# Kernel tuning notes

Measured on AMD Instinct MI355X. Metric: run time of the kernel, lower is better.

The kernel has to match this reference:

```python
import jax, jax.numpy as jnp
import numpy as np

B, S, E, H, L, DFF = 2, 2048, 512, 8, 2, 2048
D = E // H
EPS = 1e-5


def layernorm(x, g, b):
    mu = jnp.mean(x, axis=-1, keepdims=True)
    var = jnp.var(x, axis=-1, keepdims=True)
    return (x - mu) * jax.lax.rsqrt(var + EPS) * g + b


def layernorm_noaffine(x):
    mu = jnp.mean(x, axis=-1, keepdims=True)
    var = jnp.var(x, axis=-1, keepdims=True)
    return (x - mu) * jax.lax.rsqrt(var + EPS)


def setup_inputs() -> dict:
    key = jax.random.key(0)
    ks = jax.random.split(key, 16)
    s = 0.02
    inp = {
        "x": jax.random.normal(ks[0], (B, S, E), dtype=jnp.float32),
        "mask": jax.random.randint(ks[1], (B, S), 0, 2) == 1,
        # per-layer attention projections, stacked over layers
        "wq": jax.random.normal(ks[2], (L, E, E), dtype=jnp.float32) * s,
        "bq": jnp.zeros((L, E), dtype=jnp.float32),
        "wk": jax.random.normal(ks[3], (L, E, E), dtype=jnp.float32) * s,
        "bk": jnp.zeros((L, E), dtype=jnp.float32),
        "wv": jax.random.normal(ks[4], (L, E, E), dtype=jnp.float32) * s,
        "bv": jnp.zeros((L, E), dtype=jnp.float32),
        # shared norms (module defines a single norm1/norm2 used by every layer)
        "g1": jnp.ones((E,), dtype=jnp.float32),
        "b1": jnp.zeros((E,), dtype=jnp.float32),
        "g2": jnp.ones((E,), dtype=jnp.float32),
        "b2": jnp.zeros((E,), dtype=jnp.float32),
        "gf": jnp.ones((E,), dtype=jnp.float32),
        "bf": jnp.zeros((E,), dtype=jnp.float32),
        # shared Dense FFN (single self.dense used after every layer)
        "W1": jax.random.normal(ks[5], (DFF, E), dtype=jnp.float32) * s,
        "B1": jnp.zeros((DFF,), dtype=jnp.float32),
        "W2": jax.random.normal(ks[6], (E, DFF), dtype=jnp.float32) * s,
        "B2": jnp.zeros((E,), dtype=jnp.float32),
    }
    return inp


def _forward(x, wq, bq, wk, bk, wv, bv, g1, b1, g2, b2, gf, bf, W1, B1, W2, B2, mask):
    scale = 1.0 / jnp.sqrt(jnp.float32(D))
    m = mask[:, None, None, :]  # [B,1,1,S] key padding mask, True = pad
    neg_inf = jnp.float32(-jnp.inf)
    for i in range(L):
        h = layernorm(x, g1, b1)  # norm1(x), used for q,k,v
        q = (h @ wq[i].T + bq[i]).reshape(B, S, H, D).transpose(0, 2, 1, 3)
        k = (h @ wk[i].T + bk[i]).reshape(B, S, H, D).transpose(0, 2, 1, 3)
        v = (h @ wv[i].T + bv[i]).reshape(B, S, H, D).transpose(0, 2, 1, 3)
        logits = jnp.einsum("bhqd,bhkd->bhqk", q, k) * scale
        att = jax.nn.softmax(jnp.where(m, neg_inf, logits), axis=-1)
        att = jnp.where(m, 0.0, att)
        out = jnp.einsum("bhqk,bhkd->bhqd", att, v)
        out = out.transpose(0, 2, 1, 3).reshape(B, S, E)
        x = x + layernorm(out, g2, b2)
        # Dense: LayerNorm(no affine) -> Linear -> ReLU -> Linear, residual
        d = layernorm_noaffine(x)
        d = jax.nn.relu(d @ W1.T + B1)
        d = d @ W2.T + B2
        x = x + d
    return layernorm(x, gf, bf)


def reference(x, mask, wq, bq, wk, bk, wv, bv, g1, b1, g2, b2, gf, bf, W1, B1, W2, B2):
    return _forward(x, wq, bq, wk, bk, wv, bv, g1, b1, g2, b2, gf, bf, W1, B1, W2, B2, mask)
```

## Files before the change

kernel.cpp:

```cpp
#include <hip/hip_runtime.h>
#include <hip/hip_bf16.h>

constexpr int BB   = 2;
constexpr int SS   = 2048;
constexpr int EE   = 512;
constexpr int HH   = 8;
constexpr int DD   = 64;
constexpr int DFF_ = 2048;
constexpr int NTOK = BB * SS;
constexpr int NE   = NTOK * EE;
constexpr float EPSF  = 1e-5f;
constexpr float SCL2  = 0.125f * 1.44269504088896f;
constexpr float MBIAS = -1e30f;
constexpr int KSPLIT = 2;
constexpr int KHALF  = SS / KSPLIT;

typedef __bf16 v8bf __attribute__((ext_vector_type(8)));
typedef __bf16 v4bf __attribute__((ext_vector_type(4)));
typedef float  v4f  __attribute__((ext_vector_type(4)));
typedef unsigned int v4u __attribute__((ext_vector_type(4)));

__device__ __forceinline__ float bf2f(unsigned short u) {
    return __uint_as_float(((unsigned int)u) << 16);
}
__device__ __forceinline__ float bf2f(__bf16 u) {
    unsigned short us = __builtin_bit_cast(unsigned short, u);
    return __uint_as_float(((unsigned int)us) << 16);
}
__device__ __forceinline__ float ldA(const void* p, size_t i, int f) {
    return f ? ((const float*)p)[i] : bf2f(((const unsigned short*)p)[i]);
}
__device__ __forceinline__ void gll16(const void* g, void* l) {
    __builtin_amdgcn_global_load_lds(
        (const __attribute__((address_space(1))) void*)g,
        (__attribute__((address_space(3))) void*)l, 16, 0, 0);
}
__device__ __forceinline__ unsigned cvtpk(float a, float b) {
    unsigned r;
    asm("v_cvt_pk_bf16_f32 %0, %1, %2" : "=v"(r) : "v"(a), "v"(b));
    return r;
}

__global__ __launch_bounds__(256) void cvt_ln(
    const void* __restrict__ in, float* __restrict__ X,
    const void* __restrict__ g, const void* __restrict__ b,
    __bf16* __restrict__ Hb, int* __restrict__ flagw)
{
    const int row = blockIdx.x, t = threadIdx.x;
    __shared__ float red[8], st[2];
    __shared__ int scnt[4], sflag;
    {
        const unsigned short* u = (const unsigned short*)in;
        int bad = 0;
        #pragma unroll
        for (int i = 0; i < 2; ++i) {
            float v = bf2f(u[t + 256 * i]);
            if (!(fabsf(v) < 1000.f)) bad++;
        }
        #pragma unroll
        for (int off = 32; off > 0; off >>= 1) bad += __shfl_down(bad, off, 64);
        if ((t & 63) == 0) scnt[t >> 6] = bad;
        __syncthreads();
        if (t == 0) sflag = (scnt[0] + scnt[1] + scnt[2] + scnt[3] > 1) ? 1 : 0;
        __syncthreads();
    }
    const int f = sflag;
    if (row == 0 && t == 0) *flagw = f;

    const size_t i0 = (size_t)row * EE + t, i1 = i0 + 256;
    float v0 = ldA(in, i0, f);
    float v1 = ldA(in, i1, f);
    float s = v0 + v1, q = v0 * v0 + v1 * v1;
    #pragma unroll
    for (int off = 32; off > 0; off >>= 1) {
        s += __shfl_down(s, off, 64);
        q += __shfl_down(q, off, 64);
    }
    const int wid = t >> 6;
    if ((t & 63) == 0) { red[wid] = s; red[4 + wid] = q; }
    __syncthreads();
    if (t == 0) {
        float S_ = red[0] + red[1] + red[2] + red[3];
        float Q_ = red[4] + red[5] + red[6] + red[7];
        float mu = S_ / EE;
        st[0] = mu;
        st[1] = rsqrtf(Q_ / EE - mu * mu + EPSF);
    }
    __syncthreads();
    const float mu = st[0], rs = st[1];
    float o0 = (v0 - mu) * rs * ldA(g, t, f)       + ldA(b, t, f);
    float o1 = (v1 - mu) * rs * ldA(g, t + 256, f) + ldA(b, t + 256, f);
    X[i0] = v0; X[i1] = v1;
    Hb[i0] = (__bf16)o0; Hb[i1] = (__bf16)o1;
}

__global__ void wcvt_all(const void* __restrict__ wq, const void* __restrict__ wk,
                         const void* __restrict__ wv, const void* __restrict__ W1,
                         const void* __restrict__ W2, __bf16* __restrict__ out,
                         const int* __restrict__ flagp) {
    const int f = *flagp;
    const int i = (blockIdx.x * blockDim.x + threadIdx.x) * 8;
    constexpr int n1 = 2 * EE * EE;
    constexpr int nf = DFF_ * EE;
    const void* src; int off;
    if      (i < n1)          { src = wq; off = i; }
    else if (i < 2 * n1)      { src = wk; off = i - n1; }
    else if (i < 3 * n1)      { src = wv; off = i - 2 * n1; }
    else if (i < 3 * n1 + nf) { src = W1; off = i - 3 * n1; }
    else                      { src = W2; off = i - 3 * n1 - nf; }
    if (f) {
        const float* p = (const float*)src + off;
        #pragma unroll
        for (int j = 0; j < 8; ++j) out[i + j] = (__bf16)p[j];
    } else {
        *(uint4*)(out + i) = *(const uint4*)((const unsigned short*)src + off);
    }
}

__global__ __launch_bounds__(256) void ln_kernel(
    const float* __restrict__ src,
    const void* __restrict__ g, const void* __restrict__ b,
    __bf16* __restrict__ dstb, void* __restrict__ outp,
    const int* __restrict__ flagp)
{
    const int f = *flagp;
    const int row = blockIdx.x, t = threadIdx.x;
    const float* x = src + (size_t)row * EE;
    float v0 = x[t], v1 = x[t + 256];
    float s = v0 + v1, q = v0 * v0 + v1 * v1;
    #pragma unroll
    for (int off = 32; off > 0; off >>= 1) {
        s += __shfl_down(s, off, 64);
        q += __shfl_down(q, off, 64);
    }
    __shared__ float red[8], st[2];
    const int wid = t >> 6;
    if ((t & 63) == 0) { red[wid] = s; red[4 + wid] = q; }
    __syncthreads();
    if (t == 0) {
        float S_ = red[0] + red[1] + red[2] + red[3];
        float Q_ = red[4] + red[5] + red[6] + red[7];
        float mu = S_ / EE;
        st[0] = mu;
        st[1] = rsqrtf(Q_ / EE - mu * mu + EPSF);
    }
    __syncthreads();
    const float mu = st[0], rs = st[1];
    float o0 = (v0 - mu) * rs, o1 = (v1 - mu) * rs;
    if (g) {
        o0 = o0 * ldA(g, t, f)       + ldA(b, t, f);
        o1 = o1 * ldA(g, t + 256, f) + ldA(b, t + 256, f);
    }
    const size_t i0 = (size_t)row * EE + t, i1 = i0 + 256;
    if (dstb) { dstb[i0] = (__bf16)o0; dstb[i1] = (__bf16)o1; }
    if (outp) {
        if (f) { ((float*)outp)[i0] = o0; ((float*)outp)[i1] = o1; }
        else {
            ((__hip_bfloat16*)outp)[i0] = __float2bfloat16(o0);
            ((__hip_bfloat16*)outp)[i1] = __float2bfloat16(o1);
        }
    }
}

__global__ __launch_bounds__(256) void combine_ln(
    const __bf16* __restrict__ Opart, const float* __restrict__ MLl,
    const void* __restrict__ g2, const void* __restrict__ b2,
    float* __restrict__ X, __bf16* __restrict__ Hb,
    const int* __restrict__ flagp)
{
    const int f = *flagp;
    const int tok = blockIdx.x, t = threadIdx.x;
    const int b = tok >> 11, s_ = tok & 2047;
    __shared__ float cinv[8];
    __shared__ float red[8], st[2];
    if (t < 8) {
        float l = 0.f;
        #pragma unroll
        for (int zz = 0; zz < KSPLIT; ++zz)
            l += MLl[(size_t)(zz * 16 + b * 8 + t) * SS + s_];
        cinv[t] = (l > 0.f) ? 1.f / l : 0.f;
    }
    __syncthreads();
    float a0 = 0.f, a1 = 0.f;
    {
        int c = t, h = c >> 6, d = c & 63;
        #pragma unroll
        for (int zz = 0; zz < KSPLIT; ++zz)
            a0 += bf2f(Opart[((size_t)(zz * 16 + b * 8 + h) * SS + s_) * 64 + d]);
        a0 *= cinv[h];
        c = t + 256; h = c >> 6; d = c & 63;
        #pragma unroll
        for (int zz = 0; zz < KSPLIT; ++zz)
            a1 += bf2f(Opart[((size_t)(zz * 16 + b * 8 + h) * SS + s_) * 64 + d]);
        a1 *= cinv[h];
    }
    const int wid = t >> 6;
    {
        float s = a0 + a1, q = a0 * a0 + a1 * a1;
        #pragma unroll
        for (int off = 32; off > 0; off >>= 1) {
            s += __shfl_down(s, off, 64);
            q += __shfl_down(q, off, 64);
        }
        if ((t & 63) == 0) { red[wid] = s; red[4 + wid] = q; }
    }
    __syncthreads();
    if (t == 0) {
        float S_ = red[0] + red[1] + red[2] + red[3];
        float Q_ = red[4] + red[5] + red[6] + red[7];
        float mu = S_ / EE;
        st[0] = mu;
        st[1] = rsqrtf(Q_ / EE - mu * mu + EPSF);
    }
    __syncthreads();
    const float mu1 = st[0], rs1 = st[1];
    const size_t i0 = (size_t)tok * EE + t, i1 = i0 + 256;
    float l0v = (a0 - mu1) * rs1 * ldA(g2, t, f)       + ldA(b2, t, f);
    float l1v = (a1 - mu1) * rs1 * ldA(g2, t + 256, f) + ldA(b2, t + 256, f);
    float x0 = X[i0] + l0v, x1 = X[i1] + l1v;
    __syncthreads();
    {
        float s = x0 + x1, q = x0 * x0 + x1 * x1;
        #pragma unroll
        for (int off = 32; off > 0; off >>= 1) {
            s += __shfl_down(s, off, 64);
            q += __shfl_down(q, off, 64);
        }
        if ((t & 63) == 0) { red[wid] = s; red[4 + wid] = q; }
    }
    __syncthreads();
    if (t == 0) {
        float S_ = red[0] + red[1] + red[2] + red[3];
        float Q_ = red[4] + red[5] + red[6] + red[7];
        float mu = S_ / EE;
        st[0] = mu;
        st[1] = rsqrtf(Q_ / EE - mu * mu + EPSF);
    }
    __syncthreads();
    const float mu2 = st[0], rs2 = st[1];
    X[i0] = x0; X[i1] = x1;
    Hb[i0] = (__bf16)((x0 - mu2) * rs2);
    Hb[i1] = (__bf16)((x1 - mu2) * rs2);
}

__global__ __launch_bounds__(256) void gemm_mfma(
    const __bf16* __restrict__ A,
    const __bf16* Wa, const __bf16* Wb, const __bf16* Wc,
    const void* ba, const void* bb, const void* bc,
    __bf16* oa, __bf16* ob, __bf16* oc,
    float* __restrict__ Cf,
    int M, int N, int K, int flags,
    size_t welem_off, size_t belem_off, const int* __restrict__ flagp)
{
    const int f = *flagp;
    const int z = blockIdx.z;
    const __bf16* W = (z == 0) ? Wa : (z == 1) ? Wb : Wc;
    const void* bias = (z == 0) ? ba : (z == 1) ? bb : bc;
    __bf16* Cb = (z == 0) ? oa : (z == 1) ? ob : oc;
    W += welem_off;
    int kbeg = 0, kend = K;
    if (flags & 4) {
        const int ks = K >> 2;
        kbeg = z * ks; kend = kbeg + ks;
        if (z != 0) bias = nullptr;
    }

    __shared__ __bf16 As[2][128 * 64];
    __shared__ __bf16 Bs[2][128 * 64];
    const int t = threadIdx.x;
    const int w = t >> 6, lane = t & 63;
    const int quad = lane >> 4, l16 = lane & 15;
    const int wr = w >> 1, wc = w & 1;
    const int bm = blockIdx.x * 128, bn = blockIdx.y * 128;

    v4f acc[4][4] = {};

    #define STAGE_TILE(dst, src, rowbase, kk)                                   \
        _Pragma("unroll")                                                       \
        for (int ii = 0; ii < 4; ++ii) {                                        \
            const int c  = t + 256 * ii;                                        \
            const int r  = c >> 3, cc = c & 7;                                  \
            const int es = ((cc ^ (r & 7)) * 8);                                \
            gll16(src + (size_t)(rowbase + r) * K + kk + es,                    \
                  (char*)(dst) + c * 16);                                       \
        }

    STAGE_TILE(As[0], A, bm, kbeg)
    STAGE_TILE(Bs[0], W, bn, kbeg)

    int p = 0;
    for (int k0 = kbeg; k0 < kend; k0 += 64) {
        __syncthreads();
        if (k0 + 64 < kend) {
            const int kn = k0 + 64, q_ = p ^ 1;
            STAGE_TILE(As[q_], A, bm, kn)
            STAGE_TILE(Bs[q_], W, bn, kn)
        }
        #pragma unroll
        for (int ks = 0; ks < 2; ++ks) {
            v8bf af[4], bfr[4];
            #pragma unroll
            for (int i = 0; i < 4; ++i) {
                const int row = wr * 64 + i * 16 + l16;
                const int ph  = (quad + ks * 4) ^ (row & 7);
                af[i] = *(const v8bf*)&As[p][row * 64 + ph * 8];
            }
            #pragma unroll
            for (int j = 0; j < 4; ++j) {
                const int row = wc * 64 + j * 16 + l16;
                const int ph  = (quad + ks * 4) ^ (row & 7);
                bfr[j] = *(const v8bf*)&Bs[p][row * 64 + ph * 8];
            }
            #pragma unroll
            for (int i = 0; i < 4; ++i)
                #pragma unroll
                for (int j = 0; j < 4; ++j)
                    acc[i][j] = __builtin_amdgcn_mfma_f32_16x16x32_bf16(
                        af[i], bfr[j], acc[i][j], 0, 0, 0);
        }
        p ^= 1;
    }
    #undef STAGE_TILE

    float bvv[4];
    #pragma unroll
    for (int j = 0; j < 4; ++j) {
        int col = bn + wc * 64 + j * 16 + l16;
        bvv[j] = bias ? ldA(bias, belem_off + col, f) : 0.f;
    }

    #pragma unroll
    for (int i = 0; i < 4; ++i) {
        const int rowb = bm + wr * 64 + i * 16 + quad * 4;
        #pragma unroll
        for (int j = 0; j < 4; ++j) {
            const int col = bn + wc * 64 + j * 16 + l16;
            #pragma unroll
            for (int r = 0; r < 4; ++r) {
                float v = acc[i][j][r] + bvv[j];
                if (flags & 1) v = fmaxf(v, 0.f);
                const size_t idx = (size_t)(rowb + r) * N + col;
                if (flags & 4)      unsafeAtomicAdd(&Cf[idx], v);
                else if (flags & 2) Cf[idx] += v;
                else                Cb[idx] = (__bf16)v;
            }
        }
    }
}

__global__ __launch_bounds__(256) void gemm_qkv(
    const __bf16* __restrict__ A,
    const __bf16* Wa, const __bf16* Wb, const __bf16* Wc,
    const void* ba, const void* bb, const void* bc,
    __bf16* oa, __bf16* ob, __bf16* oc,
    size_t welem_off, size_t belem_off, const int* __restrict__ flagp)
{
    const int f = *flagp;
    const int z = blockIdx.z;
    const __bf16* W = (z == 0) ? Wa : (z == 1) ? Wb : Wc;
    const void* bias = (z == 0) ? ba : (z == 1) ? bb : bc;
    __bf16* Cb = (z == 0) ? oa : (z == 1) ? ob : oc;
    W += welem_off;
    constexpr int K = EE, N = EE;

    __shared__ __bf16 As[2][128 * 64];
    __shared__ __bf16 Bs[2][64 * 64];
    const int t = threadIdx.x;
    const int w = t >> 6, lane = t & 63;
    const int quad = lane >> 4, l16 = lane & 15;
    const int bm = blockIdx.x * 128, bn = blockIdx.y * 64;

    v4f acc[2][4] = {};

    #define STAGE_A(dst, kk)                                                    \
        _Pragma("unroll")                                                       \
        for (int ii = 0; ii < 4; ++ii) {                                        \
            const int c  = t + 256 * ii;                                        \
            const int r  = c >> 3, cc = c & 7;                                  \
            const int es = ((cc ^ (r & 7)) * 8);                                \
            gll16(A + (size_t)(bm + r) * K + kk + es, (char*)(dst) + c * 16);   \
        }
    #define STAGE_B(dst, kk)                                                    \
        _Pragma("unroll")                                                       \
        for (int ii = 0; ii < 2; ++ii) {                                        \
            const int c  = t + 256 * ii;                                        \
            const int r  = c >> 3, cc = c & 7;                                  \
            const int es = ((cc ^ (r & 7)) * 8);                                \
            gll16(W + (size_t)(bn + r) * K + kk + es, (char*)(dst) + c * 16);   \
        }

    STAGE_A(As[0], 0)
    STAGE_B(Bs[0], 0)

    int p = 0;
    for (int k0 = 0; k0 < K; k0 += 64) {
        __syncthreads();
        if (k0 + 64 < K) {
            const int kn = k0 + 64, q_ = p ^ 1;
            STAGE_A(As[q_], kn)
            STAGE_B(Bs[q_], kn)
        }
        #pragma unroll
        for (int ks = 0; ks < 2; ++ks) {
            v8bf af[2], bfr[4];
            #pragma unroll
            for (int i = 0; i < 2; ++i) {
                const int row = w * 32 + i * 16 + l16;
                const int ph  = (quad + ks * 4) ^ (row & 7);
                af[i] = *(const v8bf*)&As[p][row * 64 + ph * 8];
            }
            #pragma unroll
            for (int j = 0; j < 4; ++j) {
                const int row = j * 16 + l16;
                const int ph  = (quad + ks * 4) ^ (row & 7);
                bfr[j] = *(const v8bf*)&Bs[p][row * 64 + ph * 8];
            }
            #pragma unroll
            for (int i = 0; i < 2; ++i)
                #pragma unroll
                for (int j = 0; j < 4; ++j)
                    acc[i][j] = __builtin_amdgcn_mfma_f32_16x16x32_bf16(
                        af[i], bfr[j], acc[i][j], 0, 0, 0);
        }
        p ^= 1;
    }
    #undef STAGE_A
    #undef STAGE_B

    float bvv[4];
    #pragma unroll
    for (int j = 0; j < 4; ++j) {
        int col = bn + j * 16 + l16;
        bvv[j] = bias ? ldA(bias, belem_off + col, f) : 0.f;
    }

    if (z == 2) {
        #pragma unroll
        for (int i = 0; i < 2; ++i) {
            const int row0 = bm + w * 32 + i * 16 + quad * 4;
            const int b_ = row0 >> 11, sl = row0 & 2047;
            const int s64 = sl & ~63, sloc = sl & 63;
            const int slot = (sloc & 32) + ((sloc >> 2) & 3) * 8 + ((sloc >> 4) & 1) * 4;
            #pragma unroll
            for (int j = 0; j < 4; ++j) {
                const int col = bn + j * 16 + l16;
                const int h_ = col >> 6, d_ = col & 63;
                v4bf u;
                #pragma unroll
                for (int r = 0; r < 4; ++r) u[r] = (__bf16)(acc[i][j][r] + bvv[j]);
                *(v4bf*)(Cb + ((size_t)((b_ * 8 + h_) * 64 + d_)) * SS + s64 + slot) = u;
            }
        }
        return;
    }

    #pragma unroll
    for (int i = 0; i < 2; ++i) {
        const int rowb = bm + w * 32 + i * 16 + quad * 4;
        #pragma unroll
        for (int j = 0; j < 4; ++j) {
            const int col = bn + j * 16 + l16;
            #pragma unroll
            for (int r = 0; r < 4; ++r) {
                const size_t idx = (size_t)(rowb + r) * N + col;
                Cb[idx] = (__bf16)(acc[i][j][r] + bvv[j]);
            }
        }
    }
}

__global__ __launch_bounds__(256) void attn_mfma(
    const __bf16* __restrict__ Qg, const __bf16* __restrict__ Kg,
    const __bf16* __restrict__ Vtg, const int* __restrict__ mask,
    __bf16* __restrict__ Opart, float* __restrict__ MLl)
{
    __shared__ __bf16 Ks[64][72];
    __shared__ __bf16 Vs[64][72];
    __shared__ float  mkf[64];

    const int t = threadIdx.x;
    const int w = t >> 6, lane = t & 63;
    const int quad = lane >> 4, l16 = lane & 15;
    const int bh = blockIdx.y, b = bh >> 3, hh = bh & 7;
    const int q0 = blockIdx.x * 128;
    const int z  = blockIdx.z;
    const int kof = z * KHALF;

    const __bf16* qrow0 = Qg + ((size_t)(b * SS + q0 + w * 32 + l16)) * EE + hh * DD + quad * 8;
    const __bf16* qrow1 = qrow0 + (size_t)16 * EE;
    const v8bf qa00 = *(const v8bf*)qrow0;
    const v8bf qa01 = *(const v8bf*)(qrow0 + 32);
    const v8bf qa10 = *(const v8bf*)qrow1;
    const v8bf qa11 = *(const v8bf*)(qrow1 + 32);

    const int lr = t >> 2, lc = (t & 3) * 16;
    const __bf16* kbase = Kg  + ((size_t)(b * SS + kof + lr)) * EE + hh * DD + lc;
    const __bf16* vbase = Vtg + ((size_t)((b * 8 + hh) * 64 + lr)) * SS + kof + lc;

    v8bf ka0 = *(const v8bf*)kbase, ka1 = *(const v8bf*)(kbase + 8);
    v8bf va0 = *(const v8bf*)vbase, va1 = *(const v8bf*)(vbase + 8);
    float mb = 0.f;
    if (t < 64) mb = mask[b * SS + kof + t] ? MBIAS : 0.f;

    float l0 = 0.f, l1 = 0.f;
    v4f o0[4] = {}, o1[4] = {};

    #pragma unroll 1
    for (int k0 = 0; k0 < KHALF; k0 += 64) {
        *(v8bf*)&Ks[lr][lc]     = ka0;
        *(v8bf*)&Ks[lr][lc + 8] = ka1;
        *(v8bf*)&Vs[lr][lc]     = va0;
        *(v8bf*)&Vs[lr][lc + 8] = va1;
        if (t < 64) mkf[t] = mb;
        __syncthreads();
        if (k0 + 64 < KHALF) {
            ka0 = *(const v8bf*)(kbase + (size_t)(k0 + 64) * EE);
            ka1 = *(const v8bf*)(kbase + (size_t)(k0 + 64) * EE + 8);
            va0 = *(const v8bf*)(vbase + (k0 + 64));
            va1 = *(const v8bf*)(vbase + (k0 + 64) + 8);
            if (t < 64) mb = mask[b * SS + kof + k0 + 64 + t] ? MBIAS : 0.f;
        }

        v4f s0[4], s1[4];
        __builtin_amdgcn_s_setprio(1);
        #pragma unroll
        for (int j = 0; j < 4; ++j) {
            v8bf kf0 = *(const v8bf*)&Ks[j * 16 + l16][quad * 8];
            v8bf kf1 = *(const v8bf*)&Ks[j * 16 + l16][32 + quad * 8];
            v4f za = {}, zb = {};
            za = __builtin_amdgcn_mfma_f32_16x16x32_bf16(kf0, qa00, za, 0, 0, 0);
            za = __builtin_amdgcn_mfma_f32_16x16x32_bf16(kf1, qa01, za, 0, 0, 0);
            zb = __builtin_amdgcn_mfma_f32_16x16x32_bf16(kf0, qa10, zb, 0, 0, 0);
            zb = __builtin_amdgcn_mfma_f32_16x16x32_bf16(kf1, qa11, zb, 0, 0, 0);
            s0[j] = za; s1[j] = zb;
        }
        __builtin_amdgcn_s_setprio(0);
        float4 mk4[4];
        #pragma unroll
        for (int j = 0; j < 4; ++j) mk4[j] = *(const float4*)&mkf[j * 16 + quad * 4];

        float ea[16], eb[16];
        float t0 = 0.f, t1 = 0.f;
        #pragma unroll
        for (int j = 0; j < 4; ++j) {
            ea[j * 4 + 0] = exp2f(fmaf(s0[j][0], SCL2, mk4[j].x));
            ea[j * 4 + 1] = exp2f(fmaf(s0[j][1], SCL2, mk4[j].y));
            ea[j * 4 + 2] = exp2f(fmaf(s0[j][2], SCL2, mk4[j].z));
            ea[j * 4 + 3] = exp2f(fmaf(s0[j][3], SCL2, mk4[j].w));
            eb[j * 4 + 0] = exp2f(fmaf(s1[j][0], SCL2, mk4[j].x));
            eb[j * 4 + 1] = exp2f(fmaf(s1[j][1], SCL2, mk4[j].y));
            eb[j * 4 + 2] = exp2f(fmaf(s1[j][2], SCL2, mk4[j].z));
            eb[j * 4 + 3] = exp2f(fmaf(s1[j][3], SCL2, mk4[j].w));
            t0 += (ea[j * 4 + 0] + ea[j * 4 + 1]) + (ea[j * 4 + 2] + ea[j * 4 + 3]);
            t1 += (eb[j * 4 + 0] + eb[j * 4 + 1]) + (eb[j * 4 + 2] + eb[j * 4 + 3]);
        }
        l0 += t0; l1 += t1;

        v4u ua0, ua1, ub0, ub1;
        #pragma unroll
        for (int d2 = 0; d2 < 4; ++d2) {
            ua0[d2] = cvtpk(ea[d2 * 2],     ea[d2 * 2 + 1]);
            ua1[d2] = cvtpk(ea[8 + d2 * 2], ea[8 + d2 * 2 + 1]);
            ub0[d2] = cvtpk(eb[d2 * 2],     eb[d2 * 2 + 1]);
            ub1[d2] = cvtpk(eb[8 + d2 * 2], eb[8 + d2 * 2 + 1]);
        }
        const v8bf p00 = __builtin_bit_cast(v8bf, ua0);
        const v8bf p01 = __builtin_bit_cast(v8bf, ua1);
        const v8bf p10 = __builtin_bit_cast(v8bf, ub0);
        const v8bf p11 = __builtin_bit_cast(v8bf, ub1);

        __builtin_amdgcn_s_setprio(1);
        #pragma unroll
        for (int dt = 0; dt < 4; ++dt) {
            v8bf vf0 = *(const v8bf*)&Vs[dt * 16 + l16][quad * 8];
            v8bf vf1 = *(const v8bf*)&Vs[dt * 16 + l16][32 + quad * 8];
            o0[dt] = __builtin_amdgcn_mfma_f32_16x16x32_bf16(vf0, p00, o0[dt], 0, 0, 0);
            o0[dt] = __builtin_amdgcn_mfma_f32_16x16x32_bf16(vf1, p01, o0[dt], 0, 0, 0);
            o1[dt] = __builtin_amdgcn_mfma_f32_16x16x32_bf16(vf0, p10, o1[dt], 0, 0, 0);
            o1[dt] = __builtin_amdgcn_mfma_f32_16x16x32_bf16(vf1, p11, o1[dt], 0, 0, 0);
        }
        __builtin_amdgcn_s_setprio(0);
        __syncthreads();
    }

    l0 += __shfl_xor(l0, 16, 64);
    l0 += __shfl_xor(l0, 32, 64);
    l1 += __shfl_xor(l1, 16, 64);
    l1 += __shfl_xor(l1, 32, 64);

    const size_t qi0 = (size_t)(z * 16 + bh) * SS + (q0 + w * 32 + l16);
    const size_t qi1 = qi0 + 16;
    __bf16* op0 = Opart + qi0 * 64;
    __bf16* op1 = Opart + qi1 * 64;
    #pragma unroll
    for (int dt = 0; dt < 4; ++dt) {
        v4bf u0, u1;
        #pragma unroll
        for (int r = 0; r < 4; ++r) { u0[r] = (__bf16)o0[dt][r]; u1[r] = (__bf16)o1[dt][r]; }
        *(v4bf*)(op0 + dt * 16 + quad * 4) = u0;
        *(v4bf*)(op1 + dt * 16 + quad * 4) = u1;
    }
    if (quad == 0) { MLl[qi0] = l0; MLl[qi1] = l1; }
}

extern "C" void kernel_launch(void* const* d_in, const int* in_sizes, int n_in,
                              void* d_out, int out_size, void* d_ws, size_t ws_size,
                              hipStream_t stream) {
    const void* x_in = d_in[0];
    const int*  mask = (const int*)d_in[1];
    const void* wq = d_in[2];  const void* bq = d_in[3];
    const void* wk = d_in[4];  const void* bk = d_in[5];
    const void* wv = d_in[6];  const void* bv = d_in[7];
    const void* g1 = d_in[8];  const void* b1 = d_in[9];
    const void* g2 = d_in[10]; const void* b2 = d_in[11];
    const void* gf = d_in[12]; const void* bfp= d_in[13];
    const void* W1 = d_in[14]; const void* B1 = d_in[15];
    const void* W2 = d_in[16]; const void* B2 = d_in[17];

    float* base = (float*)d_ws;
    int*   flag = (int*)base;
    float* X   = base + 16;
    float* fQ  = X + NE;
    float* fK  = fQ + NE / 2;
    float* fV  = fK + NE / 2;
    float* fH  = fV + NE / 2;
    float* fW  = fH + NE / 2;
    __bf16* Qb    = (__bf16*)fQ;
    __bf16* Kb    = (__bf16*)fK;
    __bf16* Vtg   = (__bf16*)fV;
    __bf16* Hb    = (__bf16*)fH;
    __bf16* wqc = (__bf16*)fW;
    __bf16* wkc = wqc + 2 * EE * EE;
    __bf16* wvc = wkc + 2 * EE * EE;
    __bf16* W1c = wvc + 2 * EE * EE;
    __bf16* W2c = W1c + DFF_ * EE;
    float* MLl = (float*)(W2c + (size_t)EE * DFF_);
    float* fO  = MLl + (size_t)KSPLIT * 16 * SS;
    __bf16* Opart = (__bf16*)fO;
    __bf16* MID   = (__bf16*)fO;

    cvt_ln<<<NTOK, 256, 0, stream>>>(x_in, X, g1, b1, Hb, flag);
    wcvt_all<<<1792, 256, 0, stream>>>(wq, wk, wv, W1, W2, wqc, flag);

    const dim3 gQKV(NTOK / 128, EE / 64, 3);
    const dim3 gF1 (NTOK / 128, DFF_ / 128, 1);
    const dim3 gF2 (NTOK / 128, EE / 128, 4);
    const dim3 gAtt(SS / 128, BB * HH, KSPLIT);

    for (int l = 0; l < 2; ++l) {
        const size_t wo = (size_t)l * EE * EE, bo = (size_t)l * EE;
        if (l > 0)
            ln_kernel<<<NTOK, 256, 0, stream>>>(X, g1, b1, Hb, nullptr, flag);
        gemm_qkv<<<gQKV, 256, 0, stream>>>(Hb, wqc, wkc, wvc, bq, bk, bv,
            Qb, Kb, Vtg, wo, bo, flag);
        attn_mfma<<<gAtt, 256, 0, stream>>>(Qb, Kb, Vtg, mask, Opart, MLl);
        combine_ln<<<NTOK, 256, 0, stream>>>(Opart, MLl, g2, b2, X, Hb, flag);
        gemm_mfma<<<gF1, 256, 0, stream>>>(Hb, W1c, W1c, W1c, B1, B1, B1,
            MID, MID, MID, nullptr, NTOK, DFF_, EE, 1, 0, 0, flag);
        gemm_mfma<<<gF2, 256, 0, stream>>>(MID, W2c, W2c, W2c, B2, B2, B2,
            nullptr, nullptr, nullptr, X, NTOK, EE, DFF_, 2 | 4, 0, 0, flag);
    }
    ln_kernel<<<NTOK, 256, 0, stream>>>(X, gf, bfp, nullptr, d_out, flag);
}
```

Baseline: 351.8 us.

## Double-buffer K/V tiles in attention LDS and use hardware exp2

The attention kernel now keeps two LDS buffers for the K, V and mask tiles. Each iteration writes the next tile into the alternate buffer while computing on the current one, which drops one of the two barriers per iteration and overlaps the LDS stores with the MFMA work. Separately, exp2f is replaced by the amdgcn exp2 builtin, which avoids the library's range and denormal handling. The cost is double the LDS footprint per block, which could lower occupancy, plus slightly looser exp accuracy near the underflow range.

```diff
diff --git a/kernel.cpp b/kernel.cpp
--- a/kernel.cpp
+++ b/kernel.cpp
@@ -39,6 +39,13 @@
     unsigned r;
     asm("v_cvt_pk_bf16_f32 %0, %1, %2" : "=v"(r) : "v"(a), "v"(b));
     return r;
+}
+__device__ __forceinline__ float fexp2(float x) {
+#if __has_builtin(__builtin_amdgcn_exp2f)
+    return __builtin_amdgcn_exp2f(x);
+#else
+    return exp2f(x);
+#endif
 }
 
 __global__ __launch_bounds__(256) void cvt_ln(
@@ -474,9 +481,9 @@
     const __bf16* __restrict__ Vtg, const int* __restrict__ mask,
     __bf16* __restrict__ Opart, float* __restrict__ MLl)
 {
-    __shared__ __bf16 Ks[64][72];
-    __shared__ __bf16 Vs[64][72];
-    __shared__ float  mkf[64];
+    __shared__ __bf16 Ks[2][64][72];
+    __shared__ __bf16 Vs[2][64][72];
+    __shared__ float  mkf[2][64];
 
     const int t = threadIdx.x;
     const int w = t >> 6, lane = t & 63;
@@ -501,32 +508,47 @@
     v8bf va0 = *(const v8bf*)vbase, va1 = *(const v8bf*)(vbase + 8);
     float mb = 0.f;
     if (t < 64) mb = mask[b * SS + kof + t] ? MBIAS : 0.f;
+    *(v8bf*)&Ks[0][lr][lc]     = ka0;
+    *(v8bf*)&Ks[0][lr][lc + 8] = ka1;
+    *(v8bf*)&Vs[0][lr][lc]     = va0;
+    *(v8bf*)&Vs[0][lr][lc + 8] = va1;
+    if (t < 64) mkf[0][t] = mb;
+    if (64 < KHALF) {
+        ka0 = *(const v8bf*)(kbase + (size_t)64 * EE);
+        ka1 = *(const v8bf*)(kbase + (size_t)64 * EE + 8);
+        va0 = *(const v8bf*)(vbase + 64);
+        va1 = *(const v8bf*)(vbase + 64 + 8);
+        if (t < 64) mb = mask[b * SS + kof + 64 + t] ? MBIAS : 0.f;
+    }
+    __syncthreads();
 
     float l0 = 0.f, l1 = 0.f;
     v4f o0[4] = {}, o1[4] = {};
 
     #pragma unroll 1
     for (int k0 = 0; k0 < KHALF; k0 += 64) {
-        *(v8bf*)&Ks[lr][lc]     = ka0;
-        *(v8bf*)&Ks[lr][lc + 8] = ka1;
-        *(v8bf*)&Vs[lr][lc]     = va0;
-        *(v8bf*)&Vs[lr][lc + 8] = va1;
-        if (t < 64) mkf[t] = mb;
-        __syncthreads();
+        const int p = (k0 >> 6) & 1;
         if (k0 + 64 < KHALF) {
-            ka0 = *(const v8bf*)(kbase + (size_t)(k0 + 64) * EE);
-            ka1 = *(const v8bf*)(kbase + (size_t)(k0 + 64) * EE + 8);
-            va0 = *(const v8bf*)(vbase + (k0 + 64));
-            va1 = *(const v8bf*)(vbase + (k0 + 64) + 8);
-            if (t < 64) mb = mask[b * SS + kof + k0 + 64 + t] ? MBIAS : 0.f;
+            *(v8bf*)&Ks[p ^ 1][lr][lc]     = ka0;
+            *(v8bf*)&Ks[p ^ 1][lr][lc + 8] = ka1;
+            *(v8bf*)&Vs[p ^ 1][lr][lc]     = va0;
+            *(v8bf*)&Vs[p ^ 1][lr][lc + 8] = va1;
+            if (t < 64) mkf[p ^ 1][t] = mb;
+            if (k0 + 128 < KHALF) {
+                ka0 = *(const v8bf*)(kbase + (size_t)(k0 + 128) * EE);
+                ka1 = *(const v8bf*)(kbase + (size_t)(k0 + 128) * EE + 8);
+                va0 = *(const v8bf*)(vbase + (k0 + 128));
+                va1 = *(const v8bf*)(vbase + (k0 + 128) + 8);
+                if (t < 64) mb = mask[b * SS + kof + k0 + 128 + t] ? MBIAS : 0.f;
+            }
         }
 
         v4f s0[4], s1[4];
         __builtin_amdgcn_s_setprio(1);
         #pragma unroll
         for (int j = 0; j < 4; ++j) {
-            v8bf kf0 = *(const v8bf*)&Ks[j * 16 + l16][quad * 8];
-            v8bf kf1 = *(const v8bf*)&Ks[j * 16 + l16][32 + quad * 8];
+            v8bf kf0 = *(const v8bf*)&Ks[p][j * 16 + l16][quad * 8];
+            v8bf kf1 = *(const v8bf*)&Ks[p][j * 16 + l16][32 + quad * 8];
             v4f za = {}, zb = {};
             za = __builtin_amdgcn_mfma_f32_16x16x32_bf16(kf0, qa00, za, 0, 0, 0);
             za = __builtin_amdgcn_mfma_f32_16x16x32_bf16(kf1, qa01, za, 0, 0, 0);
@@ -537,20 +559,20 @@
         __builtin_amdgcn_s_setprio(0);
         float4 mk4[4];
         #pragma unroll
-        for (int j = 0; j < 4; ++j) mk4[j] = *(const float4*)&mkf[j * 16 + quad * 4];
+        for (int j = 0; j < 4; ++j) mk4[j] = *(const float4*)&mkf[p][j * 16 + quad * 4];
 
         float ea[16], eb[16];
         float t0 = 0.f, t1 = 0.f;
         #pragma unroll
         for (int j = 0; j < 4; ++j) {
-            ea[j * 4 + 0] = exp2f(fmaf(s0[j][0], SCL2, mk4[j].x));
-            ea[j * 4 + 1] = exp2f(fmaf(s0[j][1], SCL2, mk4[j].y));
-            ea[j * 4 + 2] = exp2f(fmaf(s0[j][2], SCL2, mk4[j].z));
-            ea[j * 4 + 3] = exp2f(fmaf(s0[j][3], SCL2, mk4[j].w));
-            eb[j * 4 + 0] = exp2f(fmaf(s1[j][0], SCL2, mk4[j].x));
-            eb[j * 4 + 1] = exp2f(fmaf(s1[j][1], SCL2, mk4[j].y));
-            eb[j * 4 + 2] = exp2f(fmaf(s1[j][2], SCL2, mk4[j].z));
-            eb[j * 4 + 3] = exp2f(fmaf(s1[j][3], SCL2, mk4[j].w));
+            ea[j * 4 + 0] = fexp2(fmaf(s0[j][0], SCL2, mk4[j].x));
+            ea[j * 4 + 1] = fexp2(fmaf(s0[j][1], SCL2, mk4[j].y));
+            ea[j * 4 + 2] = fexp2(fmaf(s0[j][2], SCL2, mk4[j].z));
+            ea[j * 4 + 3] = fexp2(fmaf(s0[j][3], SCL2, mk4[j].w));
+            eb[j * 4 + 0] = fexp2(fmaf(s1[j][0], SCL2, mk4[j].x));
+            eb[j * 4 + 1] = fexp2(fmaf(s1[j][1], SCL2, mk4[j].y));
+            eb[j * 4 + 2] = fexp2(fmaf(s1[j][2], SCL2, mk4[j].z));
+            eb[j * 4 + 3] = fexp2(fmaf(s1[j][3], SCL2, mk4[j].w));
             t0 += (ea[j * 4 + 0] + ea[j * 4 + 1]) + (ea[j * 4 + 2] + ea[j * 4 + 3]);
             t1 += (eb[j * 4 + 0] + eb[j * 4 + 1]) + (eb[j * 4 + 2] + eb[j * 4 + 3]);
         }
@@ -572,8 +594,8 @@
         __builtin_amdgcn_s_setprio(1);
         #pragma unroll
         for (int dt = 0; dt < 4; ++dt) {
-            v8bf vf0 = *(const v8bf*)&Vs[dt * 16 + l16][quad * 8];
-            v8bf vf1 = *(const v8bf*)&Vs[dt * 16 + l16][32 + quad * 8];
+            v8bf vf0 = *(const v8bf*)&Vs[p][dt * 16 + l16][quad * 8];
+            v8bf vf1 = *(const v8bf*)&Vs[p][dt * 16 + l16][32 + quad * 8];
             o0[dt] = __builtin_amdgcn_mfma_f32_16x16x32_bf16(vf0, p00, o0[dt], 0, 0, 0);
             o0[dt] = __builtin_amdgcn_mfma_f32_16x16x32_bf16(vf1, p01, o0[dt], 0, 0, 0);
             o1[dt] = __builtin_amdgcn_mfma_f32_16x16x32_bf16(vf0, p10, o1[dt], 0, 0, 0);
```

Result: faster. 339.7 us (median of 2 runs) (-3.4%).
